# Optimization experiments

Measured on AMD Instinct MI355X. Metric: run time of the kernel, lower is better.

## Reference

```python
import jax, jax.numpy as jnp
import numpy as np

HEADS = 8
DIM_HEAD = 64
NUM_LANDMARKS = 256
PINV_ITERS = 6
SCALE = DIM_HEAD ** -0.5
KERNEL = 33
PAD = KERNEL // 2


def moore_penrose_iter_pinv(x, iters=PINV_ITERS):
    # x: [b, h, m, m]
    abs_x = jnp.abs(x)
    col = abs_x.sum(axis=-1)
    row = abs_x.sum(axis=-2)
    # global max over all batch/head entries, as in the torch code
    z = jnp.swapaxes(x, -1, -2) / (jnp.max(col) * jnp.max(row))
    I = jnp.eye(x.shape[-1], dtype=x.dtype)
    for _ in range(iters):
        xz = x @ z
        z = 0.25 * z @ (13.0 * I - xz @ (15.0 * I - xz @ (7.0 * I - xz)))
    return z


def setup_inputs() -> dict:
    key = jax.random.key(0)
    k1, k2, k3, k4 = jax.random.split(key, 4)
    b, n, dim = 4, 4096, 512
    inner = HEADS * DIM_HEAD
    return {
        "x": jax.random.normal(k1, (b, n, dim), dtype=jnp.float32),
        "w_qkv": jax.random.normal(k2, (dim, 3 * inner), dtype=jnp.float32) * 0.02,
        "w_out": jax.random.normal(k3, (inner, dim), dtype=jnp.float32) * 0.02,
        "b_out": jnp.zeros((dim,), dtype=jnp.float32),
        "conv_w": jax.random.normal(k4, (HEADS, 1, KERNEL, 1), dtype=jnp.float32) * 0.1,
    }


def reference(x, w_qkv, w_out, b_out, conv_w):
    b, n, dim = x.shape
    h, m = HEADS, NUM_LANDMARKS
    # n is a multiple of m, so the original's left-padding branch is a no-op
    qkv = x @ w_qkv  # [b, n, 3*h*d]
    q, k, v = jnp.split(qkv, 3, axis=-1)

    def split_heads(t):
        return t.reshape(b, n, h, DIM_HEAD).transpose(0, 2, 1, 3)  # [b,h,n,d]

    q, k, v = split_heads(q), split_heads(k), split_heads(v)
    q = q * SCALE

    l = n // m  # landmark group size
    q_l = q.reshape(b, h, m, l, DIM_HEAD).mean(axis=3)  # [b,h,m,d]
    k_l = k.reshape(b, h, m, l, DIM_HEAD).mean(axis=3)

    sim1 = jnp.einsum("bhid,bhjd->bhij", q, k_l)   # [b,h,n,m]
    sim2 = jnp.einsum("bhid,bhjd->bhij", q_l, k_l)  # [b,h,m,m]
    sim3 = jnp.einsum("bhid,bhjd->bhij", q_l, k)   # [b,h,m,n]

    attn1 = jax.nn.softmax(sim1, axis=-1)
    attn2 = jax.nn.softmax(sim2, axis=-1)
    attn3 = jax.nn.softmax(sim3, axis=-1)

    attn2_inv = moore_penrose_iter_pinv(attn2, PINV_ITERS)
    out = attn1 @ (attn2_inv @ (attn3 @ v))  # [b,h,n,d]

    # residual depthwise conv along sequence dim (kernel 33x1, groups=heads)
    res = jax.lax.conv_general_dilated(
        v, conv_w,
        window_strides=(1, 1),
        padding=((PAD, PAD), (0, 0)),
        dimension_numbers=("NCHW", "OIHW", "NCHW"),
        feature_group_count=h,
    )
    out = out + res

    out = out.transpose(0, 2, 1, 3).reshape(b, n, h * DIM_HEAD)
    out = out @ w_out + b_out
    return out  # out[:, -n:] is identity since no padding was applied
```

## Files before the change

kernel.cpp:

```cpp
#include <hip/hip_runtime.h>
#include <math.h>


#define QKV_STRIDE 262144
#define LM_STRIDE 16384
#define MM_STRIDE 65536

typedef float f32x4 __attribute__((ext_vector_type(4)));
typedef short bf8 __attribute__((ext_vector_type(8)));
typedef short s4v __attribute__((ext_vector_type(4)));

__device__ __forceinline__ unsigned short f2bf_(float f) {
  unsigned u = __float_as_uint(f);
  u += 0x7FFFu + ((u >> 16) & 1u);
  return (unsigned short)(u >> 16);
}
__device__ __forceinline__ float bf2f_(unsigned short h) {
  return __uint_as_float(((unsigned)h) << 16);
}

__device__ __forceinline__ void gl16(const short* g, short* l) {
  __builtin_amdgcn_global_load_lds(
      (const __attribute__((address_space(1))) unsigned int*)g,
      (__attribute__((address_space(3))) unsigned int*)l, 16, 0, 0);
}

__global__ __launch_bounds__(256) void zero_scal(float* scal) {
  if (threadIdx.x < 2) scal[threadIdx.x] = 0.0f;
}

__global__ __launch_bounds__(256) void x_to_bf16(const float* __restrict__ x,
                                                 short* __restrict__ xb) {
  const int g = blockIdx.x * 256 + threadIdx.x;
  const float4* xp = (const float4*)x;
#pragma unroll
  for (int u = 0; u < 4; ++u) {
    const size_t i4 = (size_t)u * 524288 + g;
    float4 v = xp[i4];
    s4v o;
    o[0] = (short)f2bf_(v.x); o[1] = (short)f2bf_(v.y);
    o[2] = (short)f2bf_(v.z); o[3] = (short)f2bf_(v.w);
    *(s4v*)&xb[i4 * 4] = o;
  }
}

__global__ __launch_bounds__(256) void transpose_bf16(const float* __restrict__ src,
                                                      short* __restrict__ dst,
                                                      int R, int C) {
  __shared__ float T[32][33];
  const int t = threadIdx.x;
  const int c0 = blockIdx.x * 32, r0 = blockIdx.y * 32;
  const int tr = t >> 3, tc = (t & 7) << 2;
  float4 vsrc = *(const float4*)&src[(size_t)(r0 + tr) * C + c0 + tc];
  T[tr][tc + 0] = vsrc.x; T[tr][tc + 1] = vsrc.y;
  T[tr][tc + 2] = vsrc.z; T[tr][tc + 3] = vsrc.w;
  __syncthreads();
  s4v o;
  o[0] = (short)f2bf_(T[tc + 0][tr]);
  o[1] = (short)f2bf_(T[tc + 1][tr]);
  o[2] = (short)f2bf_(T[tc + 2][tr]);
  o[3] = (short)f2bf_(T[tc + 3][tr]);
  *(s4v*)&dst[(size_t)(c0 + tr) * R + r0 + tc] = o;
}

__global__ __launch_bounds__(256) void gemm_qkv_mfma(const short* __restrict__ xb,
                                                     const short* __restrict__ wT,
                                                     short* __restrict__ qb16,
                                                     short* __restrict__ kb16,
                                                     short* __restrict__ vT16) {
  __shared__ short SMEM[17408];
  short* As = SMEM;
  short* Bs = SMEM + 4096;
  const int tid = threadIdx.x;
  const int lane = tid & 63, w = tid >> 6;
  const int wr = w >> 1, wc = w & 1;
  const int bid = (blockIdx.x & 7) * 192 + (blockIdx.x >> 3);
  const int bn = bid % 12, bm = bid / 12;
  const int gm0 = bm * 128, gn0 = bn * 128;
  const int mA0 = (tid >> 6) * 16 + (tid & 15), kA0 = ((tid >> 4) & 3) * 8;
  const int s1 = tid + 256;
  const int mA1 = (s1 >> 6) * 16 + (s1 & 15), kA1 = ((s1 >> 4) & 3) * 8;
  const short* srcA0 = &xb[(size_t)(gm0 + mA0) * 512 + kA0];
  const short* srcA1 = &xb[(size_t)(gm0 + mA1) * 512 + kA1];
  const short* srcB0 = &wT[(size_t)(gn0 + mA0) * 512 + kA0];
  const short* srcB1 = &wT[(size_t)(gn0 + mA1) * 512 + kA1];
  short* dA0 = &As[w * 512];
  short* dA1 = &As[2048 + w * 512];
  short* dB0 = &Bs[w * 512];
  short* dB1 = &Bs[2048 + w * 512];
  f32x4 acc[4][4];
#pragma unroll
  for (int i = 0; i < 4; ++i)
#pragma unroll
    for (int j = 0; j < 4; ++j) acc[i][j] = (f32x4){0.f, 0.f, 0.f, 0.f};
  for (int kt = 0; kt < 16; ++kt) {
    const int k0 = kt * 32;
    __syncthreads();
    gl16(srcA0 + k0, dA0);
    gl16(srcA1 + k0, dA1);
    gl16(srcB0 + k0, dB0);
    gl16(srcB1 + k0, dB1);
    __syncthreads();
    bf8 af[4], bf[4];
#pragma unroll
    for (int i = 0; i < 4; ++i) {
      af[i] = *(const bf8*)&As[((wr * 4 + i) * 64 + lane) * 8];
      bf[i] = *(const bf8*)&Bs[((wc * 4 + i) * 64 + lane) * 8];
    }
#pragma unroll
    for (int i = 0; i < 4; ++i)
#pragma unroll
      for (int j = 0; j < 4; ++j)
        acc[i][j] = __builtin_amdgcn_mfma_f32_16x16x32_bf16(af[i], bf[j], acc[i][j], 0, 0, 0);
  }
  const int which = bn >> 2;
  const int qd = lane >> 4, c = lane & 15;
  if (which < 2) {
    short* dst = which == 0 ? qb16 : kb16;
    const float scale = which == 0 ? 0.125f : 1.0f;
#pragma unroll
    for (int i = 0; i < 4; ++i)
#pragma unroll
      for (int j = 0; j < 4; ++j) {
        const int col = gn0 + wc * 64 + j * 16 + c;
        const int head = (col >> 6) & 7, dd = col & 63;
#pragma unroll
        for (int r = 0; r < 4; ++r) {
          const int row = gm0 + wr * 64 + i * 16 + qd * 4 + r;
          const int b = row >> 12, seq = row & 4095;
          dst[(size_t)(b * 8 + head) * QKV_STRIDE + seq * 64 + dd] =
              (short)f2bf_(acc[i][j][r] * scale);
        }
      }
  } else {
    __syncthreads();
#pragma unroll
    for (int i = 0; i < 4; ++i)
#pragma unroll
      for (int j = 0; j < 4; ++j) {
        const int colL = wc * 64 + j * 16 + c;
#pragma unroll
        for (int r = 0; r < 4; ++r) {
          const int rowL = wr * 64 + i * 16 + qd * 4 + r;
          SMEM[colL * 136 + rowL] = (short)f2bf_(acc[i][j][r]);
        }
      }
    __syncthreads();
    const int b = gm0 >> 12, seq0 = gm0 & 4095;
    const int dcol = tid >> 1, half = tid & 1;
// ... 143 lines not shown
                                               short* __restrict__ zBhi,
                                               short* __restrict__ zBlo,
                                               short* __restrict__ zAhi,
                                               short* __restrict__ zAlo,
                                               float* __restrict__ zf) {
  const int g = blockIdx.x * 256 + threadIdx.x;
  const int j = g & 255, i = (g >> 8) & 255, bh = g >> 16;
  const float inv = 1.0f / (scal[0] * scal[1]);
  const float val = (bf2f_((unsigned short)x2hi[g]) +
                     bf2f_((unsigned short)x2lo[g])) * inv;
  const unsigned short h = f2bf_(val);
  const unsigned short lo = f2bf_(val - bf2f_(h));
  zBhi[g] = (short)h;
  zBlo[g] = (short)lo;
  const size_t tg = (size_t)bh * MM_STRIDE + (size_t)j * 256 + i;
  zAhi[tg] = (short)h;
  zAlo[tg] = (short)lo;
  zf[tg] = val;
}

__global__ __launch_bounds__(256) void pinv_mfma(const short* __restrict__ Ahi_g,
                                                 const short* __restrict__ Alo_g,
                                                 const short* __restrict__ Bhi_g,
                                                 const short* __restrict__ Blo_g,
                                                 const float* __restrict__ Ef,
                                                 float* __restrict__ Cf,
                                                 short* __restrict__ Chi,
                                                 short* __restrict__ Clo,
                                                 short* __restrict__ CThi,
                                                 short* __restrict__ CTlo,
                                                 float alpha, float beta,
                                                 int wantCf, int wantChl,
                                                 int wantT) {
  __shared__ short Ah[2048], Al[2048], Bh[2048], Bl[2048];
  __shared__ float Tbuf[64 * 68];
  const int tid = threadIdx.x;
  const int lane = tid & 63, w = tid >> 6;
  const int bid = blockIdx.x;
  const int xcd = bid & 7, y = bid >> 3;
  const int t16 = y & 15, bgrp = y >> 4;
  const int batch = bgrp * 8 + xcd;
  const int tm = t16 >> 2, tn = t16 & 3;
  const size_t bb = (size_t)batch * MM_STRIDE;
  const int ml = (tid >> 6) * 16 + (tid & 15), koff = ((tid >> 4) & 3) * 8;
  const short* sAh = Ahi_g + bb + (size_t)(tm * 64 + ml) * 256 + koff;
  const short* sAl = Alo_g + bb + (size_t)(tm * 64 + ml) * 256 + koff;
  const short* sBh = Bhi_g + bb + (size_t)(tn * 64 + ml) * 256 + koff;
  const short* sBl = Blo_g + bb + (size_t)(tn * 64 + ml) * 256 + koff;
  short* dAh = &Ah[w * 512];
  short* dAl = &Al[w * 512];
  short* dBh = &Bh[w * 512];
  short* dBl = &Bl[w * 512];
  f32x4 acc[4];
#pragma unroll
  for (int j = 0; j < 4; ++j) acc[j] = (f32x4){0.f, 0.f, 0.f, 0.f};
  for (int kt = 0; kt < 8; ++kt) {
    const int k0 = kt * 32;
    __syncthreads();
    gl16(sAh + k0, dAh);
    gl16(sAl + k0, dAl);
    gl16(sBh + k0, dBh);
    gl16(sBl + k0, dBl);
    __syncthreads();
    bf8 ah = *(const bf8*)&Ah[(w * 64 + lane) * 8];
    bf8 al = *(const bf8*)&Al[(w * 64 + lane) * 8];
#pragma unroll
    for (int j = 0; j < 4; ++j) {
      bf8 bh = *(const bf8*)&Bh[(j * 64 + lane) * 8];
      bf8 bl = *(const bf8*)&Bl[(j * 64 + lane) * 8];
      acc[j] = __builtin_amdgcn_mfma_f32_16x16x32_bf16(ah, bh, acc[j], 0, 0, 0);
      acc[j] = __builtin_amdgcn_mfma_f32_16x16x32_bf16(ah, bl, acc[j], 0, 0, 0);
      acc[j] = __builtin_amdgcn_mfma_f32_16x16x32_bf16(al, bh, acc[j], 0, 0, 0);
    }
  }
  const int qd = lane >> 4, c = lane & 15;
  float vals[4][4];
#pragma unroll
  for (int j = 0; j < 4; ++j) {
    const int col = tn * 64 + j * 16 + c;
#pragma unroll
    for (int r = 0; r < 4; ++r) {
      const int row = tm * 64 + w * 16 + qd * 4 + r;
      const size_t off = bb + (size_t)row * 256 + col;
      float e = 0.f;
      if (alpha != 0.0f) e = alpha * Ef[off];
      const float vv = e + beta * acc[j][r];
      vals[j][r] = vv;
      if (wantCf) Cf[off] = vv;
      if (wantChl) {
        const unsigned short h = f2bf_(vv);
        Chi[off] = (short)h;
        Clo[off] = (short)f2bf_(vv - bf2f_(h));
      }
    }
  }
  if (wantT) {
    __syncthreads();
#pragma unroll
    for (int j = 0; j < 4; ++j)
#pragma unroll
      for (int r = 0; r < 4; ++r)
        Tbuf[(j * 16 + c) * 68 + w * 16 + qd * 4 + r] = vals[j][r];
    __syncthreads();
    const int ctr = tid >> 2, seg = (tid & 3) * 16;
#pragma unroll
    for (int u = 0; u < 4; ++u) {
      float4 o = *(const float4*)&Tbuf[ctr * 68 + seg + u * 4];
      s4v hi, lo;
      unsigned short h;
      h = f2bf_(o.x); hi[0] = (short)h; lo[0] = (short)f2bf_(o.x - bf2f_(h));
      h = f2bf_(o.y); hi[1] = (short)h; lo[1] = (short)f2bf_(o.y - bf2f_(h));
      h = f2bf_(o.z); hi[2] = (short)h; lo[2] = (short)f2bf_(o.z - bf2f_(h));
      h = f2bf_(o.w); hi[3] = (short)h; lo[3] = (short)f2bf_(o.w - bf2f_(h));
      const size_t off = bb + (size_t)(tn * 64 + ctr) * 256 + tm * 64 + seg + u * 4;
      *(s4v*)&CThi[off] = hi;
      *(s4v*)&CTlo[off] = lo;
    }
  }
}

__global__ __launch_bounds__(256) void attn3_flash(const float* __restrict__ ql,
                                                   const short* __restrict__ kb16,
                                                   const short* __restrict__ vT16,
                                                   float* __restrict__ opart,
                                                   float* __restrict__ mpart,
                                                   float* __restrict__ lpart) {
  const int kc = blockIdx.x;
  const int rt = blockIdx.y;
  const int bh = blockIdx.z;
  __shared__ short Pa[4][4096];
  const int tid = threadIdx.x, lane = tid & 63, w = tid >> 6;
  const int qd = lane >> 4, c = lane & 15;
  const int rw = rt * 64 + w * 16;
  const float* qlp = ql + (size_t)bh * LM_STRIDE;
  const short* kp = kb16 + (size_t)bh * QKV_STRIDE;
  const short* vp = vT16 + (size_t)bh * QKV_STRIDE;
  short* Pw = &Pa[w][0];
  bf8 af[2];
#pragma unroll
  for (int st = 0; st < 2; ++st) {
    float4 x0 = *(const float4*)&qlp[(size_t)(rw + c) * 64 + st * 32 + qd * 8];
    float4 x1 = *(const float4*)&qlp[(size_t)(rw + c) * 64 + st * 32 + qd * 8 + 4];
    bf8 r;
    r[0] = (short)f2bf_(x0.x); r[1] = (short)f2bf_(x0.y);
    r[2] = (short)f2bf_(x0.z); r[3] = (short)f2bf_(x0.w);
    r[4] = (short)f2bf_(x1.x); r[5] = (short)f2bf_(x1.y);
    r[6] = (short)f2bf_(x1.z); r[7] = (short)f2bf_(x1.w);
    af[st] = r;
  }
  float m[4], l[4];
#pragma unroll
  for (int r = 0; r < 4; ++r) { m[r] = -3.0e38f; l[r] = 0.f; }
  f32x4 accO[4];
#pragma unroll
  for (int nb = 0; nb < 4; ++nb) accO[nb] = (f32x4){0.f, 0.f, 0.f, 0.f};
  for (int it = 0; it < 4; ++it) {
    const int kb0 = kc * 1024 + it * 256;
    f32x4 acc[16];
#pragma unroll
    for (int j = 0; j < 16; ++j) acc[j] = (f32x4){0.f, 0.f, 0.f, 0.f};
#pragma unroll
    for (int st = 0; st < 2; ++st)
// ... 121 lines not shown
      bf8 bhj = *(const bf8*)&ahp[(size_t)(j * 16 + c) * 256 + k0];
      bf8 blj = *(const bf8*)&alp[(size_t)(j * 16 + c) * 256 + k0];
      acc[j] = __builtin_amdgcn_mfma_f32_16x16x32_bf16(ah, bhj, acc[j], 0, 0, 0);
      acc[j] = __builtin_amdgcn_mfma_f32_16x16x32_bf16(ah, blj, acc[j], 0, 0, 0);
      acc[j] = __builtin_amdgcn_mfma_f32_16x16x32_bf16(al, bhj, acc[j], 0, 0, 0);
    }
  }
#pragma unroll
  for (int j = 0; j < 4; ++j)
#pragma unroll
    for (int r = 0; r < 4; ++r)
      Tb[(j * 16 + c) * 68 + w * 16 + qd * 4 + r] = (short)f2bf_(acc[j][r]);
  __syncthreads();
  const int col = tid >> 2, rs = (tid & 3) * 16;
  short* dst = &w2tb16[(size_t)bh * LM_STRIDE + (size_t)col * 256 + rt * 64 + rs];
  const short* srcp = &Tb[col * 68 + rs];
#pragma unroll
  for (int u = 0; u < 4; ++u) *(s4v*)&dst[u * 4] = *(const s4v*)&srcp[u * 4];
}

__global__ __launch_bounds__(256) void attn1_conv_mfma(const short* __restrict__ qb16,
                                                       const short* __restrict__ klb16,
                                                       const short* __restrict__ w2tb16,
                                                       const short* __restrict__ vT16,
                                                       const float* __restrict__ cw,
                                                       short* __restrict__ ohb16) {
  __shared__ short Pa[16384];
  __shared__ float redM[4][64], redS[4][64];
  __shared__ float rowM[64], rowI[64];
  __shared__ float cwS[33];
  const int tid = threadIdx.x;
  const int lane = tid & 63, w = tid >> 6;
  const int qd = lane >> 4, c = lane & 15;
  const int r0 = blockIdx.x * 64;
  const int bh = blockIdx.y;
  const short* qp = qb16 + (size_t)bh * QKV_STRIDE;
  const short* klp = klb16 + (size_t)bh * LM_STRIDE;
  const short* w2p = w2tb16 + (size_t)bh * LM_STRIDE;
  const short* vp = vT16 + (size_t)bh * QKV_STRIDE;

  if (tid < 33) cwS[tid] = cw[(bh & 7) * 33 + tid];

  f32x4 acc[4][4];
#pragma unroll
  for (int i = 0; i < 4; ++i)
#pragma unroll
    for (int j = 0; j < 4; ++j) acc[i][j] = (f32x4){0.f, 0.f, 0.f, 0.f};
#pragma unroll
  for (int st = 0; st < 2; ++st) {
    const int k0 = st * 32 + qd * 8;
    bf8 af[4], bf[4];
#pragma unroll
    for (int i = 0; i < 4; ++i) {
      af[i] = *(const bf8*)&qp[(size_t)(r0 + i * 16 + c) * 64 + k0];
      bf[i] = *(const bf8*)&klp[(size_t)(w * 64 + i * 16 + c) * 64 + k0];
    }
#pragma unroll
    for (int i = 0; i < 4; ++i)
#pragma unroll
      for (int j = 0; j < 4; ++j)
        acc[i][j] = __builtin_amdgcn_mfma_f32_16x16x32_bf16(af[i], bf[j], acc[i][j], 0, 0, 0);
  }
#pragma unroll
  for (int i = 0; i < 4; ++i)
#pragma unroll
    for (int r = 0; r < 4; ++r) {
      float m0 = fmaxf(fmaxf(acc[i][0][r], acc[i][1][r]),
                       fmaxf(acc[i][2][r], acc[i][3][r]));
// ... 66 lines not shown
      for (int e = 0; e < 8; ++e) {
        const int kk = kb * 32 + qd * 8 + e;
        const int t = kk - rl;
        const int s = r0 - 16 + kk;
        const float bv = (t >= 0 && t < 33 && s >= 0 && s < 4096) ? cwS[t] : 0.f;
        ba[kb][e] = (short)f2bf_(bv);
      }
    }
#pragma unroll
    for (int kb = 0; kb < 3; ++kb) {
      int s0 = r0 - 16 + kb * 32 + qd * 8;
      s0 = s0 < 0 ? 0 : (s0 > 4088 ? 4088 : s0);
#pragma unroll
      for (int nb = 0; nb < 4; ++nb) {
        bf8 bv = *(const bf8*)&vp[(size_t)(nb * 16 + c) * 4096 + s0];
        accO[nb] = __builtin_amdgcn_mfma_f32_16x16x32_bf16(ba[kb], bv, accO[nb], 0, 0, 0);
      }
    }
  }
  short* ohp = (short*)ohb16 + (size_t)bh * QKV_STRIDE;
#pragma unroll
  for (int nb = 0; nb < 4; ++nb)
#pragma unroll
    for (int r = 0; r < 4; ++r) {
      const int row = r0 + w * 16 + qd * 4 + r;
      ohp[(size_t)row * 64 + nb * 16 + c] = (short)f2bf_(accO[nb][r]);
    }
}

__global__ __launch_bounds__(256) void gemm_out_mfma(const short* __restrict__ ohb16,
                                                     const short* __restrict__ wT,
                                                     const float* __restrict__ bias,
                                                     float* __restrict__ out) {
  __shared__ short As[4096];
  __shared__ short Bs[4096];
  const int tid = threadIdx.x;
  const int lane = tid & 63, w = tid >> 6;
  const int wr = w >> 1, wc = w & 1;
  const int bid = (blockIdx.x & 7) * 64 + (blockIdx.x >> 3);
  const int bn = bid & 3, bm = bid >> 2;
  const int gm0 = bm * 128, gn0 = bn * 128;
  const int mA0 = (tid >> 6) * 16 + (tid & 15), kA0 = ((tid >> 4) & 3) * 8;
  const int s1 = tid + 256;
  const int mA1 = (s1 >> 6) * 16 + (s1 & 15), kA1 = ((s1 >> 4) & 3) * 8;
  const int b0r = (gm0 + mA0) >> 12, seq0 = (gm0 + mA0) & 4095;
  const int b1r = (gm0 + mA1) >> 12, seq1 = (gm0 + mA1) & 4095;
  short* dA0 = &As[w * 512];
  short* dA1 = &As[2048 + w * 512];
  short* dB0 = &Bs[w * 512];
  short* dB1 = &Bs[2048 + w * 512];
  f32x4 acc[4][4];
#pragma unroll
  for (int i = 0; i < 4; ++i)
#pragma unroll
    for (int j = 0; j < 4; ++j) acc[i][j] = (f32x4){0.f, 0.f, 0.f, 0.f};
  for (int kt = 0; kt < 16; ++kt) {
    const int ka = kt * 32 + kA0, kb = kt * 32 + kA1;
    __syncthreads();
    gl16(&ohb16[(size_t)(b0r * 8 + (ka >> 6)) * QKV_STRIDE + (size_t)seq0 * 64 + (ka & 63)], dA0);
    gl16(&ohb16[(size_t)(b1r * 8 + (kb >> 6)) * QKV_STRIDE + (size_t)seq1 * 64 + (kb & 63)], dA1);
    gl16(&wT[(size_t)(gn0 + mA0) * 512 + ka], dB0);
    gl16(&wT[(size_t)(gn0 + mA1) * 512 + kb], dB1);
    __syncthreads();
    bf8 af[4], bfr[4];
#pragma unroll
    for (int i = 0; i < 4; ++i) {
      af[i] = *(const bf8*)&As[((wr * 4 + i) * 64 + lane) * 8];
      bfr[i] = *(const bf8*)&Bs[((wc * 4 + i) * 64 + lane) * 8];
    }
#pragma unroll
    for (int i = 0; i < 4; ++i)
#pragma unroll
      for (int j = 0; j < 4; ++j)
        acc[i][j] = __builtin_amdgcn_mfma_f32_16x16x32_bf16(af[i], bfr[j], acc[i][j], 0, 0, 0);
  }
  const int qd = lane >> 4, c = lane & 15;
#pragma unroll
  for (int i = 0; i < 4; ++i)
#pragma unroll
    for (int j = 0; j < 4; ++j) {
      const int col = gn0 + wc * 64 + j * 16 + c;
      const float bval = bias[col];
#pragma unroll
      for (int r = 0; r < 4; ++r) {
        const int row = gm0 + wr * 64 + i * 16 + qd * 4 + r;
        out[(size_t)row * 512 + col] = acc[i][j][r] + bval;
      }
    }
}

extern "C" void kernel_launch(void* const* d_in, const int* in_sizes, int n_in,
                              void* d_out, int out_size, void* d_ws, size_t ws_size,
                              hipStream_t stream) {
  const float* x    = (const float*)d_in[0];
  const float* wqkv = (const float*)d_in[1];
  const float* wout = (const float*)d_in[2];
  const float* bout = (const float*)d_in[3];
  const float* cw   = (const float*)d_in[4];
  float* out = (float*)d_out;

  float* w = (float*)d_ws;
  short* qb16   = (short*)(w);
  short* kb16   = (short*)(w + 4194304);
  short* vT16   = (short*)(w + 8388608);
  short* xb16   = (short*)(w + 12582912);
  float* z0f    = w + 12582912;
  float* z1f    = w + 14680064;
  float* opart  = w + 12582912;
  short* ohb16  = (short*)(w + 12582912);
// ... 10 lines not shown
  short* u1Bhi  = (short*)(w + 26476544);
  short* u1Blo  = (short*)(w + 27525120);
  short* z0Ahi  = (short*)(w + 28573696);
  short* z0Alo  = (short*)(w + 29622272);
  short* z0Bhi  = (short*)(w + 30670848);
  short* z0Blo  = (short*)(w + 31719424);
  short* z1Ahi  = (short*)(w + 32768000);
  short* z1Alo  = (short*)(w + 33816576);
  short* z1Bhi  = (short*)(w + 34865152);
  short* z1Blo  = (short*)(w + 35913728);
  float* scal   = w + 36962304;
  short* wqkvT  = (short*)(w + 36962368);
  short* woutT  = (short*)(w + 37355584);
  short* avth   = (short*)(w + 20185088);
  short* avtl   = (short*)(w + 20447232);
  short* w2tb16 = (short*)(w + 20709376);
  float* mpart  = w + 26476544;
  float* lpart  = w + 26509312;

  zero_scal<<<1, 64, 0, stream>>>(scal);
  transpose_bf16<<<dim3(48, 16), 256, 0, stream>>>(wqkv, wqkvT, 512, 1536);
  transpose_bf16<<<dim3(16, 16), 256, 0, stream>>>(wout, woutT, 512, 512);
  x_to_bf16<<<2048, 256, 0, stream>>>(x, xb16);
  gemm_qkv_mfma<<<1536, 256, 0, stream>>>(xb16, wqkvT, qb16, kb16, vT16);
  lmk_mean<<<2048, 256, 0, stream>>>(qb16, kb16, ql, kl, klb16);
  sim2_softmax<<<512, 256, 0, stream>>>(ql, kl, x2hi, x2lo);
  colrow_max<<<32, 256, 0, stream>>>(x2hi, x2lo, scal);
  tscale2<<<8192, 256, 0, stream>>>(x2hi, x2lo, scal, z0Bhi, z0Blo, z0Ahi, z0Alo, z0f);

  float *zcf = z0f, *znf = z1f;
  short *zAh = z0Ahi, *zAl = z0Alo, *zBh = z0Bhi, *zBl = z0Blo;
  short *nAh = z1Ahi, *nAl = z1Alo, *nBh = z1Bhi, *nBl = z1Blo;
  for (int it = 0; it < 6; ++it) {
    pinv_mfma<<<512, 256, 0, stream>>>(x2hi, x2lo, zBh, zBl, xzf,
                                       xzf, xzAhi, xzAlo, xzBhi, xzBlo,
                                       0.f, 1.f, 1, 1, 1);
    pinv_mfma<<<512, 256, 0, stream>>>(xzAhi, xzAlo, xzBhi, xzBlo, xzf,
                                       znf, u1Bhi, u1Blo, u1Bhi, u1Blo,
                                       7.f, -1.f, 0, 0, 1);
    pinv_mfma<<<512, 256, 0, stream>>>(xzAhi, xzAlo, u1Bhi, u1Blo, xzf,
                                       znf, xzBhi, xzBlo, xzBhi, xzBlo,
                                       15.f, -1.f, 0, 0, 1);
    pinv_mfma<<<512, 256, 0, stream>>>(zAh, zAl, xzBhi, xzBlo, zcf,
                                       znf, nAh, nAl, nBh, nBl,
                                       3.25f, -0.25f, 1, 1, 1);
    float* tf = zcf; zcf = znf; znf = tf;
    short* t;
    t = zAh; zAh = nAh; nAh = t;  t = zAl; zAl = nAl; nAl = t;
    t = zBh; zBh = nBh; nBh = t;  t = zBl; zBl = nBl; nBl = t;
  }

  attn3_flash<<<dim3(4, 4, 32), 256, 0, stream>>>(ql, kb16, vT16, opart, mpart, lpart);
  attn3_merge<<<2048, 256, 0, stream>>>(opart, mpart, lpart, avth, avtl);
  zav_mfma<<<dim3(4, 32), 256, 0, stream>>>(zAh, zAl, avth, avtl, w2tb16);
  attn1_conv_mfma<<<dim3(64, 32), 256, 0, stream>>>(qb16, klb16, w2tb16, vT16, cw, ohb16);
  gemm_out_mfma<<<512, 256, 0, stream>>>(ohb16, woutT, bout, out);
}
```

Before: 801.4 us.

## Double-buffer LDS tile loads in GEMMs and swizzle block-to-batch mapping across XCDs

Converts the QKV projection, pinv, and output-projection GEMM main loops from load-sync-compute-sync into a two-stage double-buffered pipeline. The next k-tile is issued via global_load_lds while MFMAs run on the current buffer, and the loop needs one barrier per iteration instead of two. It also remaps block indices in two attention kernels so consecutive blocks spread batch-heads across the 8 XCDs, aiming for better L2 locality. The cost is twice the LDS per block, which may lower occupancy. The correctness of the single barrier relies on the async LDS loads being complete at that barrier.

```diff
diff --git a/kernel.cpp b/kernel.cpp
--- a/kernel.cpp
+++ b/kernel.cpp
@@ -69,8 +69,6 @@
                                                      short* __restrict__ kb16,
                                                      short* __restrict__ vT16) {
   __shared__ short SMEM[17408];
-  short* As = SMEM;
-  short* Bs = SMEM + 4096;
   const int tid = threadIdx.x;
   const int lane = tid & 63, w = tid >> 6;
   const int wr = w >> 1, wc = w & 1;
@@ -84,34 +82,43 @@
   const short* srcA1 = &xb[(size_t)(gm0 + mA1) * 512 + kA1];
   const short* srcB0 = &wT[(size_t)(gn0 + mA0) * 512 + kA0];
   const short* srcB1 = &wT[(size_t)(gn0 + mA1) * 512 + kA1];
-  short* dA0 = &As[w * 512];
-  short* dA1 = &As[2048 + w * 512];
-  short* dB0 = &Bs[w * 512];
-  short* dB1 = &Bs[2048 + w * 512];
   f32x4 acc[4][4];
 #pragma unroll
   for (int i = 0; i < 4; ++i)
 #pragma unroll
     for (int j = 0; j < 4; ++j) acc[i][j] = (f32x4){0.f, 0.f, 0.f, 0.f};
+  {
+    short* B0 = SMEM;
+    gl16(srcA0, B0 + w * 512);
+    gl16(srcA1, B0 + 2048 + w * 512);
+    gl16(srcB0, B0 + 4096 + w * 512);
+    gl16(srcB1, B0 + 6144 + w * 512);
+  }
+  __syncthreads();
+  int cur = 0;
   for (int kt = 0; kt < 16; ++kt) {
-    const int k0 = kt * 32;
-    __syncthreads();
-    gl16(srcA0 + k0, dA0);
-    gl16(srcA1 + k0, dA1);
-    gl16(srcB0 + k0, dB0);
-    gl16(srcB1 + k0, dB1);
-    __syncthreads();
+    if (kt < 15) {
+      short* Bn = SMEM + (cur ^ 1) * 8192;
+      const int k1 = (kt + 1) * 32;
+      gl16(srcA0 + k1, Bn + w * 512);
+      gl16(srcA1 + k1, Bn + 2048 + w * 512);
+      gl16(srcB0 + k1, Bn + 4096 + w * 512);
+      gl16(srcB1 + k1, Bn + 6144 + w * 512);
+    }
+    short* Bc = SMEM + cur * 8192;
     bf8 af[4], bf[4];
 #pragma unroll
     for (int i = 0; i < 4; ++i) {
-      af[i] = *(const bf8*)&As[((wr * 4 + i) * 64 + lane) * 8];
-      bf[i] = *(const bf8*)&Bs[((wc * 4 + i) * 64 + lane) * 8];
+      af[i] = *(const bf8*)&Bc[((wr * 4 + i) * 64 + lane) * 8];
+      bf[i] = *(const bf8*)&Bc[4096 + ((wc * 4 + i) * 64 + lane) * 8];
     }
 #pragma unroll
     for (int i = 0; i < 4; ++i)
 #pragma unroll
       for (int j = 0; j < 4; ++j)
         acc[i][j] = __builtin_amdgcn_mfma_f32_16x16x32_bf16(af[i], bf[j], acc[i][j], 0, 0, 0);
+    __syncthreads();
+    cur ^= 1;
   }
   const int which = bn >> 2;
   const int qd = lane >> 4, c = lane & 15;
@@ -324,8 +331,7 @@
                                                  float alpha, float beta,
                                                  int wantCf, int wantChl,
                                                  int wantT) {
-  __shared__ short Ah[2048], Al[2048], Bh[2048], Bl[2048];
-  __shared__ float Tbuf[64 * 68];
+  __shared__ short SM[16384];
   const int tid = threadIdx.x;
   const int lane = tid & 63, w = tid >> 6;
   const int bid = blockIdx.x;
@@ -339,32 +345,42 @@
   const short* sAl = Alo_g + bb + (size_t)(tm * 64 + ml) * 256 + koff;
   const short* sBh = Bhi_g + bb + (size_t)(tn * 64 + ml) * 256 + koff;
   const short* sBl = Blo_g + bb + (size_t)(tn * 64 + ml) * 256 + koff;
-  short* dAh = &Ah[w * 512];
-  short* dAl = &Al[w * 512];
-  short* dBh = &Bh[w * 512];
-  short* dBl = &Bl[w * 512];
   f32x4 acc[4];
 #pragma unroll
   for (int j = 0; j < 4; ++j) acc[j] = (f32x4){0.f, 0.f, 0.f, 0.f};
+  {
+    short* B0 = SM;
+    gl16(sAh, B0 + w * 512);
+    gl16(sAl, B0 + 2048 + w * 512);
+    gl16(sBh, B0 + 4096 + w * 512);
+    gl16(sBl, B0 + 6144 + w * 512);
+  }
+  __syncthreads();
+  int cur = 0;
   for (int kt = 0; kt < 8; ++kt) {
-    const int k0 = kt * 32;
-    __syncthreads();
-    gl16(sAh + k0, dAh);
-    gl16(sAl + k0, dAl);
-    gl16(sBh + k0, dBh);
-    gl16(sBl + k0, dBl);
-    __syncthreads();
-    bf8 ah = *(const bf8*)&Ah[(w * 64 + lane) * 8];
-    bf8 al = *(const bf8*)&Al[(w * 64 + lane) * 8];
+    if (kt < 7) {
+      short* Bn = SM + (cur ^ 1) * 8192;
+      const int k1 = (kt + 1) * 32;
+      gl16(sAh + k1, Bn + w * 512);
+      gl16(sAl + k1, Bn + 2048 + w * 512);
+      gl16(sBh + k1, Bn + 4096 + w * 512);
+      gl16(sBl + k1, Bn + 6144 + w * 512);
+    }
+    short* Bc = SM + cur * 8192;
+    bf8 ah = *(const bf8*)&Bc[(w * 64 + lane) * 8];
+    bf8 al = *(const bf8*)&Bc[2048 + (w * 64 + lane) * 8];
 #pragma unroll
     for (int j = 0; j < 4; ++j) {
-      bf8 bh = *(const bf8*)&Bh[(j * 64 + lane) * 8];
-      bf8 bl = *(const bf8*)&Bl[(j * 64 + lane) * 8];
+      bf8 bh = *(const bf8*)&Bc[4096 + (j * 64 + lane) * 8];
+      bf8 bl = *(const bf8*)&Bc[6144 + (j * 64 + lane) * 8];
       acc[j] = __builtin_amdgcn_mfma_f32_16x16x32_bf16(ah, bh, acc[j], 0, 0, 0);
       acc[j] = __builtin_amdgcn_mfma_f32_16x16x32_bf16(ah, bl, acc[j], 0, 0, 0);
       acc[j] = __builtin_amdgcn_mfma_f32_16x16x32_bf16(al, bh, acc[j], 0, 0, 0);
     }
-  }
+    __syncthreads();
+    cur ^= 1;
+  }
+  float* Tbuf = (float*)SM;
   const int qd = lane >> 4, c = lane & 15;
   float vals[4][4];
 #pragma unroll
@@ -417,9 +433,11 @@
                                                    float* __restrict__ opart,
                                                    float* __restrict__ mpart,
                                                    float* __restrict__ lpart) {
-  const int kc = blockIdx.x;
-  const int rt = blockIdx.y;
-  const int bh = blockIdx.z;
+  const int lin = blockIdx.z * 16 + blockIdx.y * 4 + blockIdx.x;
+  const int bh = (lin & 7) * 4 + (lin >> 7);
+  const int sub = (lin >> 3) & 15;
+  const int kc = sub >> 2;
+  const int rt = sub & 3;
   __shared__ short Pa[4][4096];
   const int tid = threadIdx.x, lane = tid & 63, w = tid >> 6;
   const int qd = lane >> 4, c = lane & 15;
@@ -607,8 +625,9 @@
   const int tid = threadIdx.x;
   const int lane = tid & 63, w = tid >> 6;
   const int qd = lane >> 4, c = lane & 15;
-  const int r0 = blockIdx.x * 64;
-  const int bh = blockIdx.y;
+  const int lin = blockIdx.y * 64 + blockIdx.x;
+  const int bh = (lin & 7) * 4 + (lin >> 9);
+  const int r0 = ((lin >> 3) & 63) * 64;
   const short* qp = qb16 + (size_t)bh * QKV_STRIDE;
   const short* klp = klb16 + (size_t)bh * LM_STRIDE;
   const short* w2p = w2tb16 + (size_t)bh * LM_STRIDE;
@@ -741,8 +760,7 @@
                                                      const short* __restrict__ wT,
                                                      const float* __restrict__ bias,
                                                      float* __restrict__ out) {
-  __shared__ short As[4096];
-  __shared__ short Bs[4096];
+  __shared__ short SMEM[16384];
   const int tid = threadIdx.x;
   const int lane = tid & 63, w = tid >> 6;
   const int wr = w >> 1, wc = w & 1;
@@ -754,34 +772,44 @@
   const int mA1 = (s1 >> 6) * 16 + (s1 & 15), kA1 = ((s1 >> 4) & 3) * 8;
   const int b0r = (gm0 + mA0) >> 12, seq0 = (gm0 + mA0) & 4095;
   const int b1r = (gm0 + mA1) >> 12, seq1 = (gm0 + mA1) & 4095;
-  short* dA0 = &As[w * 512];
-  short* dA1 = &As[2048 + w * 512];
-  short* dB0 = &Bs[w * 512];
-  short* dB1 = &Bs[2048 + w * 512];
   f32x4 acc[4][4];
 #pragma unroll
   for (int i = 0; i < 4; ++i)
 #pragma unroll
     for (int j = 0; j < 4; ++j) acc[i][j] = (f32x4){0.f, 0.f, 0.f, 0.f};
+  {
+    const int ka = kA0, kb = kA1;
+    short* B0 = SMEM;
+    gl16(&ohb16[(size_t)(b0r * 8 + (ka >> 6)) * QKV_STRIDE + (size_t)seq0 * 64 + (ka & 63)], B0 + w * 512);
+    gl16(&ohb16[(size_t)(b1r * 8 + (kb >> 6)) * QKV_STRIDE + (size_t)seq1 * 64 + (kb & 63)], B0 + 2048 + w * 512);
+    gl16(&wT[(size_t)(gn0 + mA0) * 512 + ka], B0 + 4096 + w * 512);
+    gl16(&wT[(size_t)(gn0 + mA1) * 512 + kb], B0 + 6144 + w * 512);
+  }
+  __syncthreads();
+  int cur = 0;
   for (int kt = 0; kt < 16; ++kt) {
-    const int ka = kt * 32 + kA0, kb = kt * 32 + kA1;
-    __syncthreads();
-    gl16(&ohb16[(size_t)(b0r * 8 + (ka >> 6)) * QKV_STRIDE + (size_t)seq0 * 64 + (ka & 63)], dA0);
-    gl16(&ohb16[(size_t)(b1r * 8 + (kb >> 6)) * QKV_STRIDE + (size_t)seq1 * 64 + (kb & 63)], dA1);
-    gl16(&wT[(size_t)(gn0 + mA0) * 512 + ka], dB0);
-    gl16(&wT[(size_t)(gn0 + mA1) * 512 + kb], dB1);
-    __syncthreads();
+    if (kt < 15) {
+      const int ka = (kt + 1) * 32 + kA0, kb = (kt + 1) * 32 + kA1;
+      short* Bn = SMEM + (cur ^ 1) * 8192;
+      gl16(&ohb16[(size_t)(b0r * 8 + (ka >> 6)) * QKV_STRIDE + (size_t)seq0 * 64 + (ka & 63)], Bn + w * 512);
+      gl16(&ohb16[(size_t)(b1r * 8 + (kb >> 6)) * QKV_STRIDE + (size_t)seq1 * 64 + (kb & 63)], Bn + 2048 + w * 512);
+      gl16(&wT[(size_t)(gn0 + mA0) * 512 + ka], Bn + 4096 + w * 512);
+      gl16(&wT[(size_t)(gn0 + mA1) * 512 + kb], Bn + 6144 + w * 512);
+    }
+    short* Bc = SMEM + cur * 8192;
     bf8 af[4], bfr[4];
 #pragma unroll
     for (int i = 0; i < 4; ++i) {
-      af[i] = *(const bf8*)&As[((wr * 4 + i) * 64 + lane) * 8];
-      bfr[i] = *(const bf8*)&Bs[((wc * 4 + i) * 64 + lane) * 8];
+      af[i] = *(const bf8*)&Bc[((wr * 4 + i) * 64 + lane) * 8];
+      bfr[i] = *(const bf8*)&Bc[4096 + ((wc * 4 + i) * 64 + lane) * 8];
     }
 #pragma unroll
     for (int i = 0; i < 4; ++i)
 #pragma unroll
       for (int j = 0; j < 4; ++j)
         acc[i][j] = __builtin_amdgcn_mfma_f32_16x16x32_bf16(af[i], bfr[j], acc[i][j], 0, 0, 0);
+    __syncthreads();
+    cur ^= 1;
   }
   const int qd = lane >> 4, c = lane & 15;
 #pragma unroll
```

New measurement: 812.5 us. No clear change (+1.4%).

## Load MFMA operands directly from global memory and remap blocks across XCDs

Applied to the files above, without the earlier changes.

Three GEMM kernels (QKV projection, pinv matmul, output projection) stop staging tiles in LDS through global_load_lds and barriers. Each lane now loads its bf8 MFMA fragments straight from global memory, relying on cache reuse between the waves of a block. Separately, two attention kernels linearize their block index and remap it so each batch-head's blocks spread across the XCDs. This removes LDS traffic and __syncthreads, but each operand is now fetched once per wave rather than once per block, which raises L2/global traffic and load latency with no prefetch.

```diff
diff --git a/kernel.cpp b/kernel.cpp
--- a/kernel.cpp
+++ b/kernel.cpp
@@ -17,12 +17,6 @@
 }
 __device__ __forceinline__ float bf2f_(unsigned short h) {
   return __uint_as_float(((unsigned)h) << 16);
-}
-
-__device__ __forceinline__ void gl16(const short* g, short* l) {
-  __builtin_amdgcn_global_load_lds(
-      (const __attribute__((address_space(1))) unsigned int*)g,
-      (__attribute__((address_space(3))) unsigned int*)l, 16, 0, 0);
 }
 
 __global__ __launch_bounds__(256) void zero_scal(float* scal) {
@@ -69,25 +63,15 @@
                                                      short* __restrict__ kb16,
                                                      short* __restrict__ vT16) {
   __shared__ short SMEM[17408];
-  short* As = SMEM;
-  short* Bs = SMEM + 4096;
   const int tid = threadIdx.x;
   const int lane = tid & 63, w = tid >> 6;
   const int wr = w >> 1, wc = w & 1;
+  const int qd = lane >> 4, c = lane & 15;
   const int bid = (blockIdx.x & 7) * 192 + (blockIdx.x >> 3);
   const int bn = bid % 12, bm = bid / 12;
   const int gm0 = bm * 128, gn0 = bn * 128;
-  const int mA0 = (tid >> 6) * 16 + (tid & 15), kA0 = ((tid >> 4) & 3) * 8;
-  const int s1 = tid + 256;
-  const int mA1 = (s1 >> 6) * 16 + (s1 & 15), kA1 = ((s1 >> 4) & 3) * 8;
-  const short* srcA0 = &xb[(size_t)(gm0 + mA0) * 512 + kA0];
-  const short* srcA1 = &xb[(size_t)(gm0 + mA1) * 512 + kA1];
-  const short* srcB0 = &wT[(size_t)(gn0 + mA0) * 512 + kA0];
-  const short* srcB1 = &wT[(size_t)(gn0 + mA1) * 512 + kA1];
-  short* dA0 = &As[w * 512];
-  short* dA1 = &As[2048 + w * 512];
-  short* dB0 = &Bs[w * 512];
-  short* dB1 = &Bs[2048 + w * 512];
+  const short* pxa = &xb[(size_t)(gm0 + wr * 64 + c) * 512 + qd * 8];
+  const short* pwb = &wT[(size_t)(gn0 + wc * 64 + c) * 512 + qd * 8];
   f32x4 acc[4][4];
 #pragma unroll
   for (int i = 0; i < 4; ++i)
@@ -95,17 +79,11 @@
     for (int j = 0; j < 4; ++j) acc[i][j] = (f32x4){0.f, 0.f, 0.f, 0.f};
   for (int kt = 0; kt < 16; ++kt) {
     const int k0 = kt * 32;
-    __syncthreads();
-    gl16(srcA0 + k0, dA0);
-    gl16(srcA1 + k0, dA1);
-    gl16(srcB0 + k0, dB0);
-    gl16(srcB1 + k0, dB1);
-    __syncthreads();
     bf8 af[4], bf[4];
 #pragma unroll
     for (int i = 0; i < 4; ++i) {
-      af[i] = *(const bf8*)&As[((wr * 4 + i) * 64 + lane) * 8];
-      bf[i] = *(const bf8*)&Bs[((wc * 4 + i) * 64 + lane) * 8];
+      af[i] = *(const bf8*)&pxa[i * 8192 + k0];
+      bf[i] = *(const bf8*)&pwb[i * 8192 + k0];
     }
 #pragma unroll
     for (int i = 0; i < 4; ++i)
@@ -114,7 +92,6 @@
         acc[i][j] = __builtin_amdgcn_mfma_f32_16x16x32_bf16(af[i], bf[j], acc[i][j], 0, 0, 0);
   }
   const int which = bn >> 2;
-  const int qd = lane >> 4, c = lane & 15;
   if (which < 2) {
     short* dst = which == 0 ? qb16 : kb16;
     const float scale = which == 0 ? 0.125f : 1.0f;
@@ -324,48 +301,39 @@
                                                  float alpha, float beta,
                                                  int wantCf, int wantChl,
                                                  int wantT) {
-  __shared__ short Ah[2048], Al[2048], Bh[2048], Bl[2048];
   __shared__ float Tbuf[64 * 68];
   const int tid = threadIdx.x;
   const int lane = tid & 63, w = tid >> 6;
+  const int qd = lane >> 4, c = lane & 15;
   const int bid = blockIdx.x;
   const int xcd = bid & 7, y = bid >> 3;
   const int t16 = y & 15, bgrp = y >> 4;
   const int batch = bgrp * 8 + xcd;
   const int tm = t16 >> 2, tn = t16 & 3;
   const size_t bb = (size_t)batch * MM_STRIDE;
-  const int ml = (tid >> 6) * 16 + (tid & 15), koff = ((tid >> 4) & 3) * 8;
-  const short* sAh = Ahi_g + bb + (size_t)(tm * 64 + ml) * 256 + koff;
-  const short* sAl = Alo_g + bb + (size_t)(tm * 64 + ml) * 256 + koff;
-  const short* sBh = Bhi_g + bb + (size_t)(tn * 64 + ml) * 256 + koff;
-  const short* sBl = Blo_g + bb + (size_t)(tn * 64 + ml) * 256 + koff;
-  short* dAh = &Ah[w * 512];
-  short* dAl = &Al[w * 512];
-  short* dBh = &Bh[w * 512];
-  short* dBl = &Bl[w * 512];
+  const size_t aoff = bb + (size_t)(tm * 64 + w * 16 + c) * 256 + qd * 8;
+  const size_t boff = bb + (size_t)(tn * 64 + c) * 256 + qd * 8;
+  const short* pAh = Ahi_g + aoff;
+  const short* pAl = Alo_g + aoff;
+  const short* pBh = Bhi_g + boff;
+  const short* pBl = Blo_g + boff;
   f32x4 acc[4];
 #pragma unroll
   for (int j = 0; j < 4; ++j) acc[j] = (f32x4){0.f, 0.f, 0.f, 0.f};
+#pragma unroll
   for (int kt = 0; kt < 8; ++kt) {
     const int k0 = kt * 32;
-    __syncthreads();
-    gl16(sAh + k0, dAh);
-    gl16(sAl + k0, dAl);
-    gl16(sBh + k0, dBh);
-    gl16(sBl + k0, dBl);
-    __syncthreads();
-    bf8 ah = *(const bf8*)&Ah[(w * 64 + lane) * 8];
-    bf8 al = *(const bf8*)&Al[(w * 64 + lane) * 8];
+    bf8 ah = *(const bf8*)&pAh[k0];
+    bf8 al = *(const bf8*)&pAl[k0];
 #pragma unroll
     for (int j = 0; j < 4; ++j) {
-      bf8 bh = *(const bf8*)&Bh[(j * 64 + lane) * 8];
-      bf8 bl = *(const bf8*)&Bl[(j * 64 + lane) * 8];
+      bf8 bh = *(const bf8*)&pBh[j * 4096 + k0];
+      bf8 bl = *(const bf8*)&pBl[j * 4096 + k0];
       acc[j] = __builtin_amdgcn_mfma_f32_16x16x32_bf16(ah, bh, acc[j], 0, 0, 0);
       acc[j] = __builtin_amdgcn_mfma_f32_16x16x32_bf16(ah, bl, acc[j], 0, 0, 0);
       acc[j] = __builtin_amdgcn_mfma_f32_16x16x32_bf16(al, bh, acc[j], 0, 0, 0);
     }
   }
-  const int qd = lane >> 4, c = lane & 15;
   float vals[4][4];
 #pragma unroll
   for (int j = 0; j < 4; ++j) {
@@ -417,9 +385,11 @@
                                                    float* __restrict__ opart,
                                                    float* __restrict__ mpart,
                                                    float* __restrict__ lpart) {
-  const int kc = blockIdx.x;
-  const int rt = blockIdx.y;
-  const int bh = blockIdx.z;
+  const int lin = blockIdx.z * 16 + blockIdx.y * 4 + blockIdx.x;
+  const int bh = (lin & 7) * 4 + (lin >> 7);
+  const int sub = (lin >> 3) & 15;
+  const int kc = sub >> 2;
+  const int rt = sub & 3;
   __shared__ short Pa[4][4096];
   const int tid = threadIdx.x, lane = tid & 63, w = tid >> 6;
   const int qd = lane >> 4, c = lane & 15;
@@ -607,8 +577,9 @@
   const int tid = threadIdx.x;
   const int lane = tid & 63, w = tid >> 6;
   const int qd = lane >> 4, c = lane & 15;
-  const int r0 = blockIdx.x * 64;
-  const int bh = blockIdx.y;
+  const int lin = blockIdx.y * 64 + blockIdx.x;
+  const int bh = (lin & 7) * 4 + (lin >> 9);
+  const int r0 = ((lin >> 3) & 63) * 64;
   const short* qp = qb16 + (size_t)bh * QKV_STRIDE;
   const short* klp = klb16 + (size_t)bh * LM_STRIDE;
   const short* w2p = w2tb16 + (size_t)bh * LM_STRIDE;
@@ -741,41 +712,33 @@
                                                      const short* __restrict__ wT,
                                                      const float* __restrict__ bias,
                                                      float* __restrict__ out) {
-  __shared__ short As[4096];
-  __shared__ short Bs[4096];
   const int tid = threadIdx.x;
   const int lane = tid & 63, w = tid >> 6;
   const int wr = w >> 1, wc = w & 1;
+  const int qd = lane >> 4, c = lane & 15;
   const int bid = (blockIdx.x & 7) * 64 + (blockIdx.x >> 3);
   const int bn = bid & 3, bm = bid >> 2;
   const int gm0 = bm * 128, gn0 = bn * 128;
-  const int mA0 = (tid >> 6) * 16 + (tid & 15), kA0 = ((tid >> 4) & 3) * 8;
-  const int s1 = tid + 256;
-  const int mA1 = (s1 >> 6) * 16 + (s1 & 15), kA1 = ((s1 >> 4) & 3) * 8;
-  const int b0r = (gm0 + mA0) >> 12, seq0 = (gm0 + mA0) & 4095;
-  const int b1r = (gm0 + mA1) >> 12, seq1 = (gm0 + mA1) & 4095;
-  short* dA0 = &As[w * 512];
-  short* dA1 = &As[2048 + w * 512];
-  short* dB0 = &Bs[w * 512];
-  short* dB1 = &Bs[2048 + w * 512];
+  size_t abase[4];
+#pragma unroll
+  for (int i = 0; i < 4; ++i) {
+    const int row = gm0 + wr * 64 + i * 16 + c;
+    abase[i] = (size_t)((row >> 12) * 8) * QKV_STRIDE + (size_t)(row & 4095) * 64;
+  }
+  const short* pwb = &wT[(size_t)(gn0 + wc * 64 + c) * 512 + qd * 8];
   f32x4 acc[4][4];
 #pragma unroll
   for (int i = 0; i < 4; ++i)
 #pragma unroll
     for (int j = 0; j < 4; ++j) acc[i][j] = (f32x4){0.f, 0.f, 0.f, 0.f};
   for (int kt = 0; kt < 16; ++kt) {
-    const int ka = kt * 32 + kA0, kb = kt * 32 + kA1;
-    __syncthreads();
-    gl16(&ohb16[(size_t)(b0r * 8 + (ka >> 6)) * QKV_STRIDE + (size_t)seq0 * 64 + (ka & 63)], dA0);
-    gl16(&ohb16[(size_t)(b1r * 8 + (kb >> 6)) * QKV_STRIDE + (size_t)seq1 * 64 + (kb & 63)], dA1);
-    gl16(&wT[(size_t)(gn0 + mA0) * 512 + ka], dB0);
-    gl16(&wT[(size_t)(gn0 + mA1) * 512 + kb], dB1);
-    __syncthreads();
+    const int k = kt * 32 + qd * 8;
+    const size_t koff = (size_t)(k >> 6) * QKV_STRIDE + (k & 63);
     bf8 af[4], bfr[4];
 #pragma unroll
     for (int i = 0; i < 4; ++i) {
-      af[i] = *(const bf8*)&As[((wr * 4 + i) * 64 + lane) * 8];
-      bfr[i] = *(const bf8*)&Bs[((wc * 4 + i) * 64 + lane) * 8];
+      af[i] = *(const bf8*)&ohb16[abase[i] + koff];
+      bfr[i] = *(const bf8*)&pwb[i * 8192 + kt * 32];
     }
 #pragma unroll
     for (int i = 0; i < 4; ++i)
@@ -783,7 +746,6 @@
       for (int j = 0; j < 4; ++j)
         acc[i][j] = __builtin_amdgcn_mfma_f32_16x16x32_bf16(af[i], bfr[j], acc[i][j], 0, 0, 0);
   }
-  const int qd = lane >> 4, c = lane & 15;
 #pragma unroll
   for (int i = 0; i < 4; ++i)
 #pragma unroll
```

Result: slower. 1.102 ms (+37.5%).

## Halve pinv tile width, shrink LDS, and remap block-to-XCD batch assignment

Applied to the files above, without the earlier changes.

The pinv MFMA kernel now computes 64x32 output tiles instead of 64x64, doubling the grid to 1024 blocks. Shared memory is collapsed into one 12KB buffer, with the transpose buffer aliasing the staging area, so more blocks can be resident per CU. The attn3_flash and attn1_conv kernels remap their linear block IDs so each XCD handles a contiguous set of batch-heads, aiming for better L2 locality. The trade-off is that each A tile is reloaded twice as often in pinv.

```diff
diff --git a/kernel.cpp b/kernel.cpp
--- a/kernel.cpp
+++ b/kernel.cpp
@@ -324,52 +324,52 @@
                                                  float alpha, float beta,
                                                  int wantCf, int wantChl,
                                                  int wantT) {
-  __shared__ short Ah[2048], Al[2048], Bh[2048], Bl[2048];
-  __shared__ float Tbuf[64 * 68];
+  __shared__ short SM[6144];
   const int tid = threadIdx.x;
   const int lane = tid & 63, w = tid >> 6;
-  const int bid = blockIdx.x;
-  const int xcd = bid & 7, y = bid >> 3;
-  const int t16 = y & 15, bgrp = y >> 4;
-  const int batch = bgrp * 8 + xcd;
-  const int tm = t16 >> 2, tn = t16 & 3;
+  const int qd = lane >> 4, c = lane & 15;
+  const int lin = blockIdx.x;
+  const int xcd = lin & 7;
+  const int idx = lin >> 3;
+  const int batch = xcd * 4 + (idx >> 5);
+  const int tile = idx & 31;
+  const int tm = tile >> 3;
+  const int tn = tile & 7;
   const size_t bb = (size_t)batch * MM_STRIDE;
-  const int ml = (tid >> 6) * 16 + (tid & 15), koff = ((tid >> 4) & 3) * 8;
-  const short* sAh = Ahi_g + bb + (size_t)(tm * 64 + ml) * 256 + koff;
-  const short* sAl = Alo_g + bb + (size_t)(tm * 64 + ml) * 256 + koff;
-  const short* sBh = Bhi_g + bb + (size_t)(tn * 64 + ml) * 256 + koff;
-  const short* sBl = Blo_g + bb + (size_t)(tn * 64 + ml) * 256 + koff;
-  short* dAh = &Ah[w * 512];
-  short* dAl = &Al[w * 512];
-  short* dBh = &Bh[w * 512];
-  short* dBl = &Bl[w * 512];
-  f32x4 acc[4];
-#pragma unroll
-  for (int j = 0; j < 4; ++j) acc[j] = (f32x4){0.f, 0.f, 0.f, 0.f};
+  const int arow = tm * 64 + (tid >> 6) * 16 + (tid & 15);
+  const int akk = ((tid >> 4) & 3) * 8;
+  const short* sAh = Ahi_g + bb + (size_t)arow * 256 + akk;
+  const short* sAl = Alo_g + bb + (size_t)arow * 256 + akk;
+  const int bcol = tn * 32 + ((tid >> 6) & 1) * 16 + (tid & 15);
+  const short* sB = ((tid < 128) ? Bhi_g : Blo_g) + bb + (size_t)bcol * 256 + akk;
+  short* dAh = &SM[0] + w * 512;
+  short* dAl = &SM[2048] + w * 512;
+  short* dB = &SM[4096] + w * 512;
+  f32x4 acc[2];
+#pragma unroll
+  for (int j = 0; j < 2; ++j) acc[j] = (f32x4){0.f, 0.f, 0.f, 0.f};
   for (int kt = 0; kt < 8; ++kt) {
     const int k0 = kt * 32;
     __syncthreads();
     gl16(sAh + k0, dAh);
     gl16(sAl + k0, dAl);
-    gl16(sBh + k0, dBh);
-    gl16(sBl + k0, dBl);
-    __syncthreads();
-    bf8 ah = *(const bf8*)&Ah[(w * 64 + lane) * 8];
-    bf8 al = *(const bf8*)&Al[(w * 64 + lane) * 8];
-#pragma unroll
-    for (int j = 0; j < 4; ++j) {
-      bf8 bh = *(const bf8*)&Bh[(j * 64 + lane) * 8];
-      bf8 bl = *(const bf8*)&Bl[(j * 64 + lane) * 8];
+    gl16(sB + k0, dB);
+    __syncthreads();
+    bf8 ah = *(const bf8*)&SM[(w * 64 + lane) * 8];
+    bf8 al = *(const bf8*)&SM[2048 + (w * 64 + lane) * 8];
+#pragma unroll
+    for (int j = 0; j < 2; ++j) {
+      bf8 bh = *(const bf8*)&SM[4096 + (j * 64 + lane) * 8];
+      bf8 bl = *(const bf8*)&SM[5120 + (j * 64 + lane) * 8];
       acc[j] = __builtin_amdgcn_mfma_f32_16x16x32_bf16(ah, bh, acc[j], 0, 0, 0);
       acc[j] = __builtin_amdgcn_mfma_f32_16x16x32_bf16(ah, bl, acc[j], 0, 0, 0);
       acc[j] = __builtin_amdgcn_mfma_f32_16x16x32_bf16(al, bh, acc[j], 0, 0, 0);
     }
   }
-  const int qd = lane >> 4, c = lane & 15;
-  float vals[4][4];
-#pragma unroll
-  for (int j = 0; j < 4; ++j) {
-    const int col = tn * 64 + j * 16 + c;
+  float vals[2][4];
+#pragma unroll
+  for (int j = 0; j < 2; ++j) {
+    const int col = tn * 32 + j * 16 + c;
 #pragma unroll
     for (int r = 0; r < 4; ++r) {
       const int row = tm * 64 + w * 16 + qd * 4 + r;
@@ -387,16 +387,17 @@
     }
   }
   if (wantT) {
-    __syncthreads();
-#pragma unroll
-    for (int j = 0; j < 4; ++j)
+    float* Tbuf = (float*)SM;
+    __syncthreads();
+#pragma unroll
+    for (int j = 0; j < 2; ++j)
 #pragma unroll
       for (int r = 0; r < 4; ++r)
         Tbuf[(j * 16 + c) * 68 + w * 16 + qd * 4 + r] = vals[j][r];
     __syncthreads();
-    const int ctr = tid >> 2, seg = (tid & 3) * 16;
-#pragma unroll
-    for (int u = 0; u < 4; ++u) {
+    const int ctr = tid >> 3, seg = (tid & 7) * 8;
+#pragma unroll
+    for (int u = 0; u < 2; ++u) {
       float4 o = *(const float4*)&Tbuf[ctr * 68 + seg + u * 4];
       s4v hi, lo;
       unsigned short h;
@@ -404,7 +405,7 @@
       h = f2bf_(o.y); hi[1] = (short)h; lo[1] = (short)f2bf_(o.y - bf2f_(h));
       h = f2bf_(o.z); hi[2] = (short)h; lo[2] = (short)f2bf_(o.z - bf2f_(h));
       h = f2bf_(o.w); hi[3] = (short)h; lo[3] = (short)f2bf_(o.w - bf2f_(h));
-      const size_t off = bb + (size_t)(tn * 64 + ctr) * 256 + tm * 64 + seg + u * 4;
+      const size_t off = bb + (size_t)(tn * 32 + ctr) * 256 + tm * 64 + seg + u * 4;
       *(s4v*)&CThi[off] = hi;
       *(s4v*)&CTlo[off] = lo;
     }
@@ -417,9 +418,11 @@
                                                    float* __restrict__ opart,
                                                    float* __restrict__ mpart,
                                                    float* __restrict__ lpart) {
-  const int kc = blockIdx.x;
-  const int rt = blockIdx.y;
-  const int bh = blockIdx.z;
+  const int lin = blockIdx.z * 16 + blockIdx.y * 4 + blockIdx.x;
+  const int bh = (lin & 7) * 4 + (lin >> 7);
+  const int sub = (lin >> 3) & 15;
+  const int kc = sub >> 2;
+  const int rt = sub & 3;
   __shared__ short Pa[4][4096];
   const int tid = threadIdx.x, lane = tid & 63, w = tid >> 6;
   const int qd = lane >> 4, c = lane & 15;
@@ -607,8 +610,9 @@
   const int tid = threadIdx.x;
   const int lane = tid & 63, w = tid >> 6;
   const int qd = lane >> 4, c = lane & 15;
-  const int r0 = blockIdx.x * 64;
-  const int bh = blockIdx.y;
+  const int lin = blockIdx.y * 64 + blockIdx.x;
+  const int bh = (lin & 7) * 4 + (lin >> 9);
+  const int r0 = ((lin >> 3) & 63) * 64;
   const short* qp = qb16 + (size_t)bh * QKV_STRIDE;
   const short* klp = klb16 + (size_t)bh * LM_STRIDE;
   const short* w2p = w2tb16 + (size_t)bh * LM_STRIDE;
@@ -860,18 +864,18 @@
   short *zAh = z0Ahi, *zAl = z0Alo, *zBh = z0Bhi, *zBl = z0Blo;
   short *nAh = z1Ahi, *nAl = z1Alo, *nBh = z1Bhi, *nBl = z1Blo;
   for (int it = 0; it < 6; ++it) {
-    pinv_mfma<<<512, 256, 0, stream>>>(x2hi, x2lo, zBh, zBl, xzf,
-                                       xzf, xzAhi, xzAlo, xzBhi, xzBlo,
-                                       0.f, 1.f, 1, 1, 1);
-    pinv_mfma<<<512, 256, 0, stream>>>(xzAhi, xzAlo, xzBhi, xzBlo, xzf,
-                                       znf, u1Bhi, u1Blo, u1Bhi, u1Blo,
-                                       7.f, -1.f, 0, 0, 1);
-    pinv_mfma<<<512, 256, 0, stream>>>(xzAhi, xzAlo, u1Bhi, u1Blo, xzf,
-                                       znf, xzBhi, xzBlo, xzBhi, xzBlo,
-                                       15.f, -1.f, 0, 0, 1);
-    pinv_mfma<<<512, 256, 0, stream>>>(zAh, zAl, xzBhi, xzBlo, zcf,
-                                       znf, nAh, nAl, nBh, nBl,
-                                       3.25f, -0.25f, 1, 1, 1);
+    pinv_mfma<<<1024, 256, 0, stream>>>(x2hi, x2lo, zBh, zBl, xzf,
+                                        xzf, xzAhi, xzAlo, xzBhi, xzBlo,
+                                        0.f, 1.f, 1, 1, 1);
+    pinv_mfma<<<1024, 256, 0, stream>>>(xzAhi, xzAlo, xzBhi, xzBlo, xzf,
+                                        znf, u1Bhi, u1Blo, u1Bhi, u1Blo,
+                                        7.f, -1.f, 0, 0, 1);
+    pinv_mfma<<<1024, 256, 0, stream>>>(xzAhi, xzAlo, u1Bhi, u1Blo, xzf,
+                                        znf, xzBhi, xzBlo, xzBhi, xzBlo,
+                                        15.f, -1.f, 0, 0, 1);
+    pinv_mfma<<<1024, 256, 0, stream>>>(zAh, zAl, xzBhi, xzBlo, zcf,
+                                        znf, nAh, nAl, nBh, nBl,
+                                        3.25f, -0.25f, 1, 1, 1);
     float* tf = zcf; zcf = znf; znf = tf;
     short* t;
     t = zAh; zAh = nAh; nAh = t;  t = zAl; zAl = nAl; nAl = t;
```

Result: slower. 848.0 us (+5.8%).
